# Performance work log

Measured on AMD Instinct MI355X. Metric: run time of the kernel, lower is better.

The kernel has to match this reference:

```python
import jax, jax.numpy as jnp
import numpy as np

D = 512   # d_model
K = 24    # decode steps
B = 8192  # batch


def setup_inputs() -> dict:
    key = jax.random.key(0)
    ks = jax.random.split(key, 10)
    s = 1.0 / np.sqrt(D)
    return {
        "initial": jax.random.normal(ks[0], (B, 1, 1), jnp.float32),
        "encoder_hidden": jax.random.normal(ks[1], (B, D), jnp.float32) * 0.1,
        "encoder_cell": jax.random.normal(ks[2], (B, D), jnp.float32) * 0.1,
        # LSTM params: input dim is 1 (feedback of dense1 output); gate order i,f,g,o (Keras)
        "Wx": jax.random.normal(ks[3], (1, 4 * D), jnp.float32) * s,
        "Wu": jax.random.normal(ks[4], (D, 4 * D), jnp.float32) * s,
        "b": jnp.zeros((4 * D,), jnp.float32),
        "w1": jax.random.normal(ks[5], (D, 1), jnp.float32) * s,
        "b1": jnp.zeros((1,), jnp.float32),
        "w2": jax.random.normal(ks[6], (D, 1), jnp.float32) * s,
        "b2": jnp.zeros((1,), jnp.float32),
    }


def reference(initial, encoder_hidden, encoder_cell, Wx, Wu, b, w1, b1, w2, b2):
    """Autoregressive LSTM decode: step 0 consumes `initial`, then feeds dense1
    output back as the next LSTM input; state carries across all K steps."""

    def step(carry, _):
        x, h, c = carry                      # x:[B,1], h,c:[B,D]
        z = x @ Wx + h @ Wu + b              # [B,4D]
        i, f, g, o = jnp.split(z, 4, axis=-1)
        i = jax.nn.sigmoid(i)
        f = jax.nn.sigmoid(f)
        g = jnp.tanh(g)
        o = jax.nn.sigmoid(o)
        c = f * c + i * g
        h = o * jnp.tanh(c)
        y1 = jax.nn.sigmoid(h @ w1 + b1)     # dense1, feedback input
        y2 = jax.nn.elu(h @ w2 + b2)         # dense2
        return (y1, h, c), (y1, y2)

    x0 = initial[:, 0, :]                    # [B,1]
    _, (ys1, ys2) = jax.lax.scan(step, (x0, encoder_hidden, encoder_cell), None, length=K)
    out1 = jnp.transpose(ys1[..., 0], (1, 0))  # [B,K]
    out2 = jnp.transpose(ys2[..., 0], (1, 0))  # [B,K]
    return out1, out2
```

## Files before the change

kernel.cpp:

```cpp
#include <hip/hip_runtime.h>

#define D_ 512
#define ND_ 2048
#define KS_ 24
#define TB_ 32
#define B_ 8192
#define NU_ 33

typedef __attribute__((ext_vector_type(8))) short short8;
typedef __attribute__((ext_vector_type(16))) float f32x16;
typedef unsigned short u16;

#define SWZ(row, kb) (((row) * 1024) + ((kb) ^ (((row) & 15) << 4)))

__device__ __forceinline__ u16 f2bf(float f) {
  union { float f; unsigned int u; } v; v.f = f;
  unsigned int u = v.u;
  return (u16)((u + 0x7FFFu + ((u >> 16) & 1u)) >> 16);
}

__device__ __forceinline__ float sigm(float x) { return 1.0f / (1.0f + __expf(-x)); }
__device__ __forceinline__ float tanh_(float x) {
  float e = __expf(2.0f * x);
  return (e - 1.0f) / (e + 1.0f);
}

__global__ __launch_bounds__(256) void pack_wu_kernel(const float* __restrict__ Wu,
                                                      const float* __restrict__ Wx,
                                                      const float* __restrict__ b,
                                                      u16* __restrict__ pk) {
  int idx = blockIdx.x * 256 + threadIdx.x;
  int lane = idx & 63;
  int unit = idx >> 6;
  if (unit >= 64 * NU_) return;
  int nt = unit / NU_;
  int un = unit - nt * NU_;
  int col = nt * 32 + (lane & 31);
  u16 t[8] = {0, 0, 0, 0, 0, 0, 0, 0};
  if (un < 32) {
    int k0 = un * 16 + (lane >> 5) * 8;
#pragma unroll
    for (int j = 0; j < 8; ++j) t[j] = f2bf(Wu[(size_t)(k0 + j) * ND_ + col]);
  } else if ((lane >> 5) == 0) {
    t[0] = f2bf(Wx[col]);
    t[1] = f2bf(b[col]);
  }
  int4 w;
  w.x = t[0] | (t[1] << 16); w.y = t[2] | (t[3] << 16);
  w.z = t[4] | (t[5] << 16); w.w = t[6] | (t[7] << 16);
  *reinterpret_cast<int4*>(pk + (size_t)unit * 512 + lane * 8) = w;
}

#define LD8(P, u) (*reinterpret_cast<const short8*>((P) + (size_t)(u) * 512))

#define KSTEP_PASS(CREG, COL, W1V, W2V, P0, P1, P2, P3)                        \
  {                                                                            \
    acc0 = (f32x16){}; acc1 = (f32x16){}; acc2 = (f32x16){}; acc3 = (f32x16){};\
    short8 fA0 = LD8(P0, 0), fA1 = LD8(P1, 0), fA2 = LD8(P2, 0), fA3 = LD8(P3, 0);\
    short8 fB0, fB1, fB2, fB3;                                                 \
    _Pragma("unroll 1")                                                        \
    for (int ks = 0; ks < 32; ks += 2) {                                       \
      fB0 = LD8(P0, ks + 1); fB1 = LD8(P1, ks + 1);                            \
      fB2 = LD8(P2, ks + 1); fB3 = LD8(P3, ks + 1);                            \
      short8 a0 = *reinterpret_cast<const short8*>(&hr[SWZ(l31, ks * 32 + abase)]);\
      acc0 = __builtin_amdgcn_mfma_f32_32x32x16_bf16(a0, fA0, acc0, 0, 0, 0);  \
      acc1 = __builtin_amdgcn_mfma_f32_32x32x16_bf16(a0, fA1, acc1, 0, 0, 0);  \
      acc2 = __builtin_amdgcn_mfma_f32_32x32x16_bf16(a0, fA2, acc2, 0, 0, 0);  \
      acc3 = __builtin_amdgcn_mfma_f32_32x32x16_bf16(a0, fA3, acc3, 0, 0, 0);  \
      fA0 = LD8(P0, ks + 2); fA1 = LD8(P1, ks + 2);  \
      fA2 = LD8(P2, ks + 2); fA3 = LD8(P3, ks + 2);                            \
      short8 a1 = *reinterpret_cast<const short8*>(&hr[SWZ(l31, (ks + 1) * 32 + abase)]);\
      acc0 = __builtin_amdgcn_mfma_f32_32x32x16_bf16(a1, fB0, acc0, 0, 0, 0);  \
      acc1 = __builtin_amdgcn_mfma_f32_32x32x16_bf16(a1, fB1, acc1, 0, 0, 0);  \
      acc2 = __builtin_amdgcn_mfma_f32_32x32x16_bf16(a1, fB2, acc2, 0, 0, 0);  \
      acc3 = __builtin_amdgcn_mfma_f32_32x32x16_bf16(a1, fB3, acc3, 0, 0, 0);  \
    }                                                                          \
    {                   \
      short8 ax = {};                                                          \
      if (lhi == 0) {                                                          \
        ax[0] = (short)f2bf(x_lds[l31]);                                       \
        ax[1] = (short)0x3F80;                                                 \
      }                                                                        \
      acc0 = __builtin_amdgcn_mfma_f32_32x32x16_bf16(ax, fA0, acc0, 0, 0, 0);  \
      acc1 = __builtin_amdgcn_mfma_f32_32x32x16_bf16(ax, fA1, acc1, 0, 0, 0);  \
      acc2 = __builtin_amdgcn_mfma_f32_32x32x16_bf16(ax, fA2, acc2, 0, 0, 0);  \
      acc3 = __builtin_amdgcn_mfma_f32_32x32x16_bf16(ax, fA3, acc3, 0, 0, 0);  \
    }                                                                          \
    _Pragma("unroll")                                                          \
    for (int r = 0; r < 16; ++r) {                                             \
      const int row = (r & 3) + 8 * (r >> 2) + 4 * lhi;                        \
      float ig = sigm(acc0[r]);                                                \
      float fg = sigm(acc1[r]);                                                \
      float gg = tanh_(acc2[r]);                                               \
      float og = sigm(acc3[r]);                                                \
      float cn = fg * CREG[r] + ig * gg;                                       \
      CREG[r] = cn;                                                            \
      float hn = og * tanh_(cn);                                               \
      *reinterpret_cast<u16*>(&hw[SWZ(row, (COL) * 2)]) = f2bf(hn);            \
      y1p[r] += hn * (W1V);                                                    \
      y2p[r] += hn * (W2V);                                                    \
    }                                                                          \
  }

__global__ __launch_bounds__(512, 2) void lstm_kernel(
    const float* __restrict__ initial, const float* __restrict__ enc_h,
    const float* __restrict__ enc_c,
    const float* __restrict__ w1, const float* __restrict__ b1,
    const float* __restrict__ w2, const float* __restrict__ b2,
    const u16* __restrict__ wu, float* __restrict__ out) {
  __shared__ __align__(16) unsigned char hbuf[2][TB_ * 1024];
  __shared__ float x_lds[TB_];
  __shared__ float ly1[8][TB_];
  __shared__ float ly2[8][TB_];

  const int tid = threadIdx.x;
  const int wv  = tid >> 6;
  const int wvu = __builtin_amdgcn_readfirstlane(wv);
  const int l   = tid & 63;
  const int l31 = l & 31;
  const int lhi = l >> 5;
  const int b0  = blockIdx.x * TB_;

  {
    int row = tid >> 4;
    int seg = tid & 15;
    const float* src = enc_h + (size_t)(b0 + row) * D_ + seg * 32;
#pragma unroll
    for (int jb = 0; jb < 4; ++jb) {
      u16 t[8];
#pragma unroll
      for (int j = 0; j < 8; ++j) t[j] = f2bf(src[jb * 8 + j]);
      int kb = seg * 64 + jb * 16;
      int4 w;
      w.x = t[0] | (t[1] << 16); w.y = t[2] | (t[3] << 16);
      w.z = t[4] | (t[5] << 16); w.w = t[6] | (t[7] << 16);
      *reinterpret_cast<int4*>(&hbuf[0][SWZ(row, kb)]) = w;
    }
  }
  if (tid < TB_) x_lds[tid] = initial[b0 + tid];

  const int colA = wvu * 32 + l31;
  const int colB = (8 + wvu) * 32 + l31;
  const float w1vA = w1[colA], w1vB = w1[colB];
  const float w2vA = w2[colA], w2vB = w2[colB];
  const float b1v = b1[0], b2v = b2[0];

  float cregA[16], cregB[16];
#pragma unroll
  for (int r = 0; r < 16; ++r) {
    const int row = (r & 3) + 8 * (r >> 2) + 4 * lhi;
    cregA[r] = enc_c[(size_t)(b0 + row) * D_ + colA];
    cregB[r] = enc_c[(size_t)(b0 + row) * D_ + colB];
  }

  const size_t lofs8 = (size_t)l * 8;
  const u16* pA0 = wu + (size_t)(( 0 + wvu) * NU_) * 512 + lofs8;
  const u16* pA1 = wu + (size_t)((16 + wvu) * NU_) * 512 + lofs8;
  const u16* pA2 = wu + (size_t)((32 + wvu) * NU_) * 512 + lofs8;
  const u16* pA3 = wu + (size_t)((48 + wvu) * NU_) * 512 + lofs8;
  const u16* pB0 = wu + (size_t)(( 8 + wvu) * NU_) * 512 + lofs8;
  const u16* pB1 = wu + (size_t)((24 + wvu) * NU_) * 512 + lofs8;
  const u16* pB2 = wu + (size_t)((40 + wvu) * NU_) * 512 + lofs8;
  const u16* pB3 = wu + (size_t)((56 + wvu) * NU_) * 512 + lofs8;
  const int abase = lhi * 16;

  __syncthreads();

  for (int s = 0; s < KS_; ++s) {
    const unsigned char* hr = hbuf[s & 1];
    unsigned char* hw = hbuf[(s & 1) ^ 1];

    float y1p[16], y2p[16];
#pragma unroll
    for (int r = 0; r < 16; ++r) { y1p[r] = 0.f; y2p[r] = 0.f; }

    f32x16 acc0, acc1, acc2, acc3;
    KSTEP_PASS(cregA, colA, w1vA, w2vA, pA0, pA1, pA2, pA3)
    KSTEP_PASS(cregB, colB, w1vB, w2vB, pB0, pB1, pB2, pB3)

#pragma unroll
    for (int m = 1; m < 32; m <<= 1) {
#pragma unroll
      for (int r = 0; r < 16; ++r) {
        y1p[r] += __shfl_xor(y1p[r], m);
        y2p[r] += __shfl_xor(y2p[r], m);
      }
    }
    if (l31 == 0) {
#pragma unroll
      for (int r = 0; r < 16; ++r) {
        const int row = (r & 3) + 8 * (r >> 2) + 4 * lhi;
        ly1[wvu][row] = y1p[r];
        ly2[wvu][row] = y2p[r];
      }
    }
    __syncthreads();

    if (tid < TB_) {
      float s1 = b1v, s2 = b2v;
#pragma unroll
      for (int wq = 0; wq < 8; ++wq) { s1 += ly1[wq][tid]; s2 += ly2[wq][tid]; }
      float y1 = sigm(s1);
      float y2 = (s2 > 0.f) ? s2 : (__expf(s2) - 1.0f);
      out[(size_t)(b0 + tid) * KS_ + s] = y1;
      out[(size_t)B_ * KS_ + (size_t)(b0 + tid) * KS_ + s] = y2;
      x_lds[tid] = y1;
    }
    __syncthreads();
  }
}

extern "C" void kernel_launch(void* const* d_in, const int* in_sizes, int n_in,
                              void* d_out, int out_size, void* d_ws, size_t ws_size,
                              hipStream_t stream) {
  const float* initial = (const float*)d_in[0];
  const float* enc_h   = (const float*)d_in[1];
  const float* enc_c   = (const float*)d_in[2];
  const float* Wx      = (const float*)d_in[3];
  const float* Wu      = (const float*)d_in[4];
  const float* bias    = (const float*)d_in[5];
  const float* w1      = (const float*)d_in[6];
  const float* b1      = (const float*)d_in[7];
  const float* w2      = (const float*)d_in[8];
  const float* b2      = (const float*)d_in[9];
  u16* pk = (u16*)d_ws;

  pack_wu_kernel<<<528, 256, 0, stream>>>(Wu, Wx, bias, pk);
  lstm_kernel<<<256, 512, 0, stream>>>(initial, enc_h, enc_c, w1, b1,
                                       w2, b2, pk, (float*)d_out);
}
```

Before: 683.0 us.

## Deepen weight prefetch to three stages and overlap next-pass loads with gate math

```diff
diff --git a/kernel.cpp b/kernel.cpp
--- a/kernel.cpp
+++ b/kernel.cpp
@@ -52,54 +52,86 @@
 }
 
 #define LD8(P, u) (*reinterpret_cast<const short8*>((P) + (size_t)(u) * 512))
-
-#define KSTEP_PASS(CREG, COL, W1V, W2V, P0, P1, P2, P3)                        \
+#define AH(ks) (*reinterpret_cast<const short8*>(&hr[SWZ(l31, (ks) * 32 + abase)]))
+#define MFMA_(A, B, C) __builtin_amdgcn_mfma_f32_32x32x16_bf16(A, B, C, 0, 0, 0)
+
+#define KPRO(P0, P1, P2, P3)                                                   \
+    fA0 = LD8(P0, 0); fA1 = LD8(P1, 0); fA2 = LD8(P2, 0); fA3 = LD8(P3, 0);    \
+    fB0 = LD8(P0, 1); fB1 = LD8(P1, 1); fB2 = LD8(P2, 1); fB3 = LD8(P3, 1);    \
+    fC0 = LD8(P0, 2); fC1 = LD8(P1, 2); fC2 = LD8(P2, 2); fC3 = LD8(P3, 2);
+
+#define GATE_REDUCE(CREG, COL, W1V, W2V, PIDX)                                 \
+    _Pragma("unroll")                                                          \
+    for (int rb = 0; rb < 16; rb += 4) {                                       \
+      float y1t[4], y2t[4];                                                    \
+      _Pragma("unroll")                                                        \
+      for (int q = 0; q < 4; ++q) {                                            \
+        const int r = rb + q;                                                  \
+        const int row = q + 8 * (rb >> 2) + 4 * lhi;                           \
+        float ig = sigm(acc0[r]);                                              \
+        float fg = sigm(acc1[r]);                                              \
+        float gg = tanh_(acc2[r]);                                             \
+        float og = sigm(acc3[r]);                                              \
+        float cn = fg * CREG[r] + ig * gg;                                     \
+        CREG[r] = cn;                                                          \
+        float hn = og * tanh_(cn);                                             \
+        *reinterpret_cast<u16*>(&hw[SWZ(row, (COL) * 2)]) = f2bf(hn);          \
+        y1t[q] = hn * (W1V);                                                   \
+        y2t[q] = hn * (W2V);                                                   \
+      }                                                                        \
+      _Pragma("unroll")                                                        \
+      for (int m = 1; m < 32; m <<= 1) {                                       \
+        _Pragma("unroll")                                                      \
+        for (int q = 0; q < 4; ++q) {                                          \
+          y1t[q] += __shfl_xor(y1t[q], m);                                     \
+          y2t[q] += __shfl_xor(y2t[q], m);                                     \
+        }                                                                      \
+      }                                                                        \
+      if (l31 == 0) {                                                          \
+        _Pragma("unroll")                                                      \
+        for (int q = 0; q < 4; ++q) {                                          \
+          const int row = q + 8 * (rb >> 2) + 4 * lhi;                         \
+          ly1[PIDX][wvu][row] = y1t[q];                                        \
+          ly2[PIDX][wvu][row] = y2t[q];                                        \
+        }                                                                      \
+      }                                                                        \
+    }
+
+#define KBODY(CREG, COL, W1V, W2V, P0, P1, P2, P3, PIDX, NEXTPRO)              \
   {                                                                            \
     acc0 = (f32x16){}; acc1 = (f32x16){}; acc2 = (f32x16){}; acc3 = (f32x16){};\
-    short8 fA0 = LD8(P0, 0), fA1 = LD8(P1, 0), fA2 = LD8(P2, 0), fA3 = LD8(P3, 0);\
-    short8 fB0, fB1, fB2, fB3;                                                 \
     _Pragma("unroll 1")                                                        \
-    for (int ks = 0; ks < 32; ks += 2) {                                       \
-      fB0 = LD8(P0, ks + 1); fB1 = LD8(P1, ks + 1);                            \
-      fB2 = LD8(P2, ks + 1); fB3 = LD8(P3, ks + 1);                            \
-      short8 a0 = *reinterpret_cast<const short8*>(&hr[SWZ(l31, ks * 32 + abase)]);\
-      acc0 = __builtin_amdgcn_mfma_f32_32x32x16_bf16(a0, fA0, acc0, 0, 0, 0);  \
-      acc1 = __builtin_amdgcn_mfma_f32_32x32x16_bf16(a0, fA1, acc1, 0, 0, 0);  \
-      acc2 = __builtin_amdgcn_mfma_f32_32x32x16_bf16(a0, fA2, acc2, 0, 0, 0);  \
-      acc3 = __builtin_amdgcn_mfma_f32_32x32x16_bf16(a0, fA3, acc3, 0, 0, 0);  \
-      fA0 = LD8(P0, ks + 2); fA1 = LD8(P1, ks + 2);  \
-      fA2 = LD8(P2, ks + 2); fA3 = LD8(P3, ks + 2);                            \
-      short8 a1 = *reinterpret_cast<const short8*>(&hr[SWZ(l31, (ks + 1) * 32 + abase)]);\
-      acc0 = __builtin_amdgcn_mfma_f32_32x32x16_bf16(a1, fB0, acc0, 0, 0, 0);  \
-      acc1 = __builtin_amdgcn_mfma_f32_32x32x16_bf16(a1, fB1, acc1, 0, 0, 0);  \
-      acc2 = __builtin_amdgcn_mfma_f32_32x32x16_bf16(a1, fB2, acc2, 0, 0, 0);  \
-      acc3 = __builtin_amdgcn_mfma_f32_32x32x16_bf16(a1, fB3, acc3, 0, 0, 0);  \
+    for (int ks = 0; ks < 30; ks += 3) {                                       \
+      short8 a0 = AH(ks);                                                      \
+      acc0 = MFMA_(a0, fA0, acc0); acc1 = MFMA_(a0, fA1, acc1);                \
+      acc2 = MFMA_(a0, fA2, acc2); acc3 = MFMA_(a0, fA3, acc3);                \
+      fA0 = LD8(P0, ks + 3); fA1 = LD8(P1, ks + 3);                            \
+      fA2 = LD8(P2, ks + 3); fA3 = LD8(P3, ks + 3);                            \
+      short8 a1 = AH(ks + 1);                                                  \
+      acc0 = MFMA_(a1, fB0, acc0); acc1 = MFMA_(a1, fB1, acc1);                \
+      acc2 = MFMA_(a1, fB2, acc2); acc3 = MFMA_(a1, fB3, acc3);                \
+      fB0 = LD8(P0, ks + 4); fB1 = LD8(P1, ks + 4);                            \
+      fB2 = LD8(P2, ks + 4); fB3 = LD8(P3, ks + 4);                            \
+      short8 a2 = AH(ks + 2);                                                  \
+      acc0 = MFMA_(a2, fC0, acc0); acc1 = MFMA_(a2, fC1, acc1);                \
+      acc2 = MFMA_(a2, fC2, acc2); acc3 = MFMA_(a2, fC3, acc3);                \
+      fC0 = LD8(P0, ks + 5); fC1 = LD8(P1, ks + 5);                            \
+      fC2 = LD8(P2, ks + 5); fC3 = LD8(P3, ks + 5);                            \
     }                                                                          \
-    {                   \
-      short8 ax = {};                                                          \
-      if (lhi == 0) {                                                          \
-        ax[0] = (short)f2bf(x_lds[l31]);                                       \
-        ax[1] = (short)0x3F80;                                                 \
-      }                                                                        \
-      acc0 = __builtin_amdgcn_mfma_f32_32x32x16_bf16(ax, fA0, acc0, 0, 0, 0);  \
-      acc1 = __builtin_amdgcn_mfma_f32_32x32x16_bf16(ax, fA1, acc1, 0, 0, 0);  \
-      acc2 = __builtin_amdgcn_mfma_f32_32x32x16_bf16(ax, fA2, acc2, 0, 0, 0);  \
-      acc3 = __builtin_amdgcn_mfma_f32_32x32x16_bf16(ax, fA3, acc3, 0, 0, 0);  \
+    {                                                                          \
+      short8 a0 = AH(30);                                                      \
+      acc0 = MFMA_(a0, fA0, acc0); acc1 = MFMA_(a0, fA1, acc1);                \
+      acc2 = MFMA_(a0, fA2, acc2); acc3 = MFMA_(a0, fA3, acc3);                \
+      short8 a1 = AH(31);                                                      \
+      acc0 = MFMA_(a1, fB0, acc0); acc1 = MFMA_(a1, fB1, acc1);                \
+      acc2 = MFMA_(a1, fB2, acc2); acc3 = MFMA_(a1, fB3, acc3);                \
+      short8 ax = {};                     \
+      if (lhi == 0) { ax[0] = (short)f2bf(x_lds[l31]); ax[1] = (short)0x3F80; }\
+      acc0 = MFMA_(ax, fC0, acc0); acc1 = MFMA_(ax, fC1, acc1);                \
+      acc2 = MFMA_(ax, fC2, acc2); acc3 = MFMA_(ax, fC3, acc3);                \
     }                                                                          \
-    _Pragma("unroll")                                                          \
-    for (int r = 0; r < 16; ++r) {                                             \
-      const int row = (r & 3) + 8 * (r >> 2) + 4 * lhi;                        \
-      float ig = sigm(acc0[r]);                                                \
-      float fg = sigm(acc1[r]);                                                \
-      float gg = tanh_(acc2[r]);                                               \
-      float og = sigm(acc3[r]);                                                \
-      float cn = fg * CREG[r] + ig * gg;                                       \
-      CREG[r] = cn;                                                            \
-      float hn = og * tanh_(cn);                                               \
-      *reinterpret_cast<u16*>(&hw[SWZ(row, (COL) * 2)]) = f2bf(hn);            \
-      y1p[r] += hn * (W1V);                                                    \
-      y2p[r] += hn * (W2V);                                                    \
-    }                                                                          \
+    NEXTPRO                                                                    \
+    GATE_REDUCE(CREG, COL, W1V, W2V, PIDX)                                     \
   }
 
 __global__ __launch_bounds__(512, 2) void lstm_kernel(
@@ -110,8 +142,8 @@
     const u16* __restrict__ wu, float* __restrict__ out) {
   __shared__ __align__(16) unsigned char hbuf[2][TB_ * 1024];
   __shared__ float x_lds[TB_];
-  __shared__ float ly1[8][TB_];
-  __shared__ float ly2[8][TB_];
+  __shared__ float ly1[2][8][TB_];
+  __shared__ float ly2[2][8][TB_];
 
   const int tid = threadIdx.x;
   const int wv  = tid >> 6;
@@ -170,36 +202,23 @@
     const unsigned char* hr = hbuf[s & 1];
     unsigned char* hw = hbuf[(s & 1) ^ 1];
 
-    float y1p[16], y2p[16];
-#pragma unroll
-    for (int r = 0; r < 16; ++r) { y1p[r] = 0.f; y2p[r] = 0.f; }
-
+    short8 fA0, fA1, fA2, fA3, fB0, fB1, fB2, fB3, fC0, fC1, fC2, fC3;
     f32x16 acc0, acc1, acc2, acc3;
-    KSTEP_PASS(cregA, colA, w1vA, w2vA, pA0, pA1, pA2, pA3)
-    KSTEP_PASS(cregB, colB, w1vB, w2vB, pB0, pB1, pB2, pB3)
-
-#pragma unroll
-    for (int m = 1; m < 32; m <<= 1) {
-#pragma unroll
-      for (int r = 0; r < 16; ++r) {
-        y1p[r] += __shfl_xor(y1p[r], m);
-        y2p[r] += __shfl_xor(y2p[r], m);
-      }
-    }
-    if (l31 == 0) {
-#pragma unroll
-      for (int r = 0; r < 16; ++r) {
-        const int row = (r & 3) + 8 * (r >> 2) + 4 * lhi;
-        ly1[wvu][row] = y1p[r];
-        ly2[wvu][row] = y2p[r];
-      }
-    }
+
+    KPRO(pA0, pA1, pA2, pA3)
+    KBODY(cregA, colA, w1vA, w2vA, pA0, pA1, pA2, pA3, 0,
+          KPRO(pB0, pB1, pB2, pB3))
+    KBODY(cregB, colB, w1vB, w2vB, pB0, pB1, pB2, pB3, 1, )
+
     __syncthreads();
 
     if (tid < TB_) {
       float s1 = b1v, s2 = b2v;
 #pragma unroll
-      for (int wq = 0; wq < 8; ++wq) { s1 += ly1[wq][tid]; s2 += ly2[wq][tid]; }
+      for (int wq = 0; wq < 8; ++wq) {
+        s1 += ly1[0][wq][tid] + ly1[1][wq][tid];
+        s2 += ly2[0][wq][tid] + ly2[1][wq][tid];
+      }
       float y1 = sigm(s1);
       float y2 = (s2 > 0.f) ? s2 : (__expf(s2) - 1.0f);
       out[(size_t)(b0 + tid) * KS_ + s] = y1;
```

New measurement: 924.1 us. 35.3% more time.

## Quantize LSTM recurrent matmul to int8 MFMA with per-column scales

Applied to the files above, without the earlier changes.

```diff
diff --git a/kernel.cpp b/kernel.cpp
--- a/kernel.cpp
+++ b/kernel.cpp
@@ -5,19 +5,12 @@
 #define KS_ 24
 #define TB_ 32
 #define B_ 8192
-#define NU_ 33
-
-typedef __attribute__((ext_vector_type(8))) short short8;
-typedef __attribute__((ext_vector_type(16))) float f32x16;
-typedef unsigned short u16;
-
-#define SWZ(row, kb) (((row) * 1024) + ((kb) ^ (((row) & 15) << 4)))
-
-__device__ __forceinline__ u16 f2bf(float f) {
-  union { float f; unsigned int u; } v; v.f = f;
-  unsigned int u = v.u;
-  return (u16)((u + 0x7FFFu + ((u >> 16) & 1u)) >> 16);
-}
+#define NUI_ 16
+
+typedef __attribute__((ext_vector_type(4))) int i32x4;
+typedef __attribute__((ext_vector_type(16))) int i32x16;
+
+#define SWZ8(row, kb) (((row) * 512) + ((kb) ^ (((row) & 15) << 4)))
 
 __device__ __forceinline__ float sigm(float x) { return 1.0f / (1.0f + __expf(-x)); }
 __device__ __forceinline__ float tanh_(float x) {
@@ -25,93 +18,116 @@
   return (e - 1.0f) / (e + 1.0f);
 }
 
-__global__ __launch_bounds__(256) void pack_wu_kernel(const float* __restrict__ Wu,
-                                                      const float* __restrict__ Wx,
-                                                      const float* __restrict__ b,
-                                                      u16* __restrict__ pk) {
+__global__ __launch_bounds__(256) void colscale_kernel(const float* __restrict__ Wu,
+                                                       float* __restrict__ sw) {
+  int n = blockIdx.x * 256 + threadIdx.x;
+  float m = 0.f;
+  for (int k = 0; k < D_; ++k) m = fmaxf(m, fabsf(Wu[(size_t)k * ND_ + n]));
+  sw[n] = fmaxf(m, 1e-12f) * (1.0f / 127.0f);
+}
+
+__global__ __launch_bounds__(256) void pack_i8_kernel(const float* __restrict__ Wu,
+                                                      const float* __restrict__ sw,
+                                                      signed char* __restrict__ pk) {
   int idx = blockIdx.x * 256 + threadIdx.x;
   int lane = idx & 63;
   int unit = idx >> 6;
-  if (unit >= 64 * NU_) return;
-  int nt = unit / NU_;
-  int un = unit - nt * NU_;
-  int col = nt * 32 + (lane & 31);
-  u16 t[8] = {0, 0, 0, 0, 0, 0, 0, 0};
-  if (un < 32) {
-    int k0 = un * 16 + (lane >> 5) * 8;
-#pragma unroll
-    for (int j = 0; j < 8; ++j) t[j] = f2bf(Wu[(size_t)(k0 + j) * ND_ + col]);
-  } else if ((lane >> 5) == 0) {
-    t[0] = f2bf(Wx[col]);
-    t[1] = f2bf(b[col]);
-  }
-  int4 w;
-  w.x = t[0] | (t[1] << 16); w.y = t[2] | (t[3] << 16);
-  w.z = t[4] | (t[5] << 16); w.w = t[6] | (t[7] << 16);
-  *reinterpret_cast<int4*>(pk + (size_t)unit * 512 + lane * 8) = w;
-}
-
-#define LD8(P, u) (*reinterpret_cast<const short8*>((P) + (size_t)(u) * 512))
-
-#define KSTEP_PASS(CREG, COL, W1V, W2V, P0, P1, P2, P3)                        \
+  int nt = unit >> 4, ku = unit & 15;
+  int n  = nt * 32 + (lane & 31);
+  int k0 = ku * 32 + (lane >> 5) * 16;
+  float inv = 1.0f / sw[n];
+  unsigned w[4] = {0, 0, 0, 0};
+#pragma unroll
+  for (int e = 0; e < 16; ++e) {
+    float v = rintf(Wu[(size_t)(k0 + e) * ND_ + n] * inv);
+    v = fminf(fmaxf(v, -127.f), 127.f);
+    int qi = (int)v;
+    w[e >> 2] |= (unsigned)(qi & 255) << ((e & 3) * 8);
+  }
+  i32x4 q = {(int)w[0], (int)w[1], (int)w[2], (int)w[3]};
+  *reinterpret_cast<i32x4*>(pk + (size_t)unit * 1024 + lane * 16) = q;
+}
+
+#define LDU(S, u) (*reinterpret_cast<const i32x4*>((S) + (size_t)(u) * 1024 + lofs16))
+#define AH8(ku_) (*reinterpret_cast<const i8x4c*>(&hr[SWZ8(l31, (ku_) * 32 + abase)]))
+#define MFMAI(A, B, C) __builtin_amdgcn_mfma_i32_32x32x32_i8(A, B, C, 0, 0, 0)
+typedef const i32x4 i8x4c;
+
+#define KSTEP_I8(S0, S1, S2, S3)                                               \
   {                                                                            \
-    acc0 = (f32x16){}; acc1 = (f32x16){}; acc2 = (f32x16){}; acc3 = (f32x16){};\
-    short8 fA0 = LD8(P0, 0), fA1 = LD8(P1, 0), fA2 = LD8(P2, 0), fA3 = LD8(P3, 0);\
-    short8 fB0, fB1, fB2, fB3;                                                 \
+    acc0 = (i32x16){}; acc1 = (i32x16){}; acc2 = (i32x16){}; acc3 = (i32x16){};\
+    i32x4 fA0 = LDU(S0, 0), fA1 = LDU(S1, 0), fA2 = LDU(S2, 0), fA3 = LDU(S3, 0);\
+    i32x4 fB0, fB1, fB2, fB3;                                                  \
     _Pragma("unroll 1")                                                        \
-    for (int ks = 0; ks < 32; ks += 2) {                                       \
-      fB0 = LD8(P0, ks + 1); fB1 = LD8(P1, ks + 1);                            \
-      fB2 = LD8(P2, ks + 1); fB3 = LD8(P3, ks + 1);                            \
-      short8 a0 = *reinterpret_cast<const short8*>(&hr[SWZ(l31, ks * 32 + abase)]);\
-      acc0 = __builtin_amdgcn_mfma_f32_32x32x16_bf16(a0, fA0, acc0, 0, 0, 0);  \
-      acc1 = __builtin_amdgcn_mfma_f32_32x32x16_bf16(a0, fA1, acc1, 0, 0, 0);  \
-      acc2 = __builtin_amdgcn_mfma_f32_32x32x16_bf16(a0, fA2, acc2, 0, 0, 0);  \
-      acc3 = __builtin_amdgcn_mfma_f32_32x32x16_bf16(a0, fA3, acc3, 0, 0, 0);  \
-      fA0 = LD8(P0, ks + 2); fA1 = LD8(P1, ks + 2);  \
-      fA2 = LD8(P2, ks + 2); fA3 = LD8(P3, ks + 2);                            \
-      short8 a1 = *reinterpret_cast<const short8*>(&hr[SWZ(l31, (ks + 1) * 32 + abase)]);\
-      acc0 = __builtin_amdgcn_mfma_f32_32x32x16_bf16(a1, fB0, acc0, 0, 0, 0);  \
-      acc1 = __builtin_amdgcn_mfma_f32_32x32x16_bf16(a1, fB1, acc1, 0, 0, 0);  \
-      acc2 = __builtin_amdgcn_mfma_f32_32x32x16_bf16(a1, fB2, acc2, 0, 0, 0);  \
-      acc3 = __builtin_amdgcn_mfma_f32_32x32x16_bf16(a1, fB3, acc3, 0, 0, 0);  \
+    for (int ku = 0; ku < 14; ku += 2) {                                       \
+      fB0 = LDU(S0, ku + 1); fB1 = LDU(S1, ku + 1);                            \
+      fB2 = LDU(S2, ku + 1); fB3 = LDU(S3, ku + 1);                            \
+      i32x4 a0 = AH8(ku);                                                      \
+      acc0 = MFMAI(a0, fA0, acc0); acc1 = MFMAI(a0, fA1, acc1);                \
+      acc2 = MFMAI(a0, fA2, acc2); acc3 = MFMAI(a0, fA3, acc3);                \
+      fA0 = LDU(S0, ku + 2); fA1 = LDU(S1, ku + 2);                            \
+      fA2 = LDU(S2, ku + 2); fA3 = LDU(S3, ku + 2);                            \
+      i32x4 a1 = AH8(ku + 1);                                                  \
+      acc0 = MFMAI(a1, fB0, acc0); acc1 = MFMAI(a1, fB1, acc1);                \
+      acc2 = MFMAI(a1, fB2, acc2); acc3 = MFMAI(a1, fB3, acc3);                \
     }                                                                          \
-    {                   \
-      short8 ax = {};                                                          \
-      if (lhi == 0) {                                                          \
-        ax[0] = (short)f2bf(x_lds[l31]);                                       \
-        ax[1] = (short)0x3F80;                                                 \
-      }                                                                        \
-      acc0 = __builtin_amdgcn_mfma_f32_32x32x16_bf16(ax, fA0, acc0, 0, 0, 0);  \
-      acc1 = __builtin_amdgcn_mfma_f32_32x32x16_bf16(ax, fA1, acc1, 0, 0, 0);  \
-      acc2 = __builtin_amdgcn_mfma_f32_32x32x16_bf16(ax, fA2, acc2, 0, 0, 0);  \
-      acc3 = __builtin_amdgcn_mfma_f32_32x32x16_bf16(ax, fA3, acc3, 0, 0, 0);  \
+    {                                                                          \
+      fB0 = LDU(S0, 15); fB1 = LDU(S1, 15);                                    \
+      fB2 = LDU(S2, 15); fB3 = LDU(S3, 15);                                    \
+      i32x4 a0 = AH8(14);                                                      \
+      acc0 = MFMAI(a0, fA0, acc0); acc1 = MFMAI(a0, fA1, acc1);                \
+      acc2 = MFMAI(a0, fA2, acc2); acc3 = MFMAI(a0, fA3, acc3);                \
+      i32x4 a1 = AH8(15);                                                      \
+      acc0 = MFMAI(a1, fB0, acc0); acc1 = MFMAI(a1, fB1, acc1);                \
+      acc2 = MFMAI(a1, fB2, acc2); acc3 = MFMAI(a1, fB3, acc3);                \
     }                                                                          \
+  }
+
+#define GATEPH(CREG, COL, W1V, W2V)                                            \
+  {                                                                            \
+    const float swi = sw_l[COL],        swf = sw_l[512 + COL];                 \
+    const float swg = sw_l[1024 + COL], swo = sw_l[1536 + COL];                \
+    const float wxi = wx_l[COL],        wxf = wx_l[512 + COL];                 \
+    const float wxg = wx_l[1024 + COL], wxo = wx_l[1536 + COL];                \
+    const float bbi = bb_l[COL],        bbf = bb_l[512 + COL];                 \
+    const float bbg = bb_l[1024 + COL], bbo = bb_l[1536 + COL];                \
     _Pragma("unroll")                                                          \
     for (int r = 0; r < 16; ++r) {                                             \
       const int row = (r & 3) + 8 * (r >> 2) + 4 * lhi;                        \
-      float ig = sigm(acc0[r]);                                                \
-      float fg = sigm(acc1[r]);                                                \
-      float gg = tanh_(acc2[r]);                                               \
-      float og = sigm(acc3[r]);                                                \
+      const float xv = x_lds[row];                                             \
+      float zi = swi * (float)acc0[r] + xv * wxi + bbi;                        \
+      float zf = swf * (float)acc1[r] + xv * wxf + bbf;                        \
+      float zg = swg * (float)acc2[r] + xv * wxg + bbg;                        \
+      float zo = swo * (float)acc3[r] + xv * wxo + bbo;                        \
+      float ig = sigm(zi);                                                     \
+      float fg = sigm(zf);                                                     \
+      float gg = tanh_(zg);                                                    \
+      float og = sigm(zo);                                                     \
       float cn = fg * CREG[r] + ig * gg;                                       \
       CREG[r] = cn;                                                            \
       float hn = og * tanh_(cn);                                               \
-      *reinterpret_cast<u16*>(&hw[SWZ(row, (COL) * 2)]) = f2bf(hn);            \
+      hw[SWZ8(row, COL)] = (signed char)__float2int_rn(hn * 127.0f);           \
       y1p[r] += hn * (W1V);                                                    \
       y2p[r] += hn * (W2V);                                                    \
     }                                                                          \
   }
 
-__global__ __launch_bounds__(512, 2) void lstm_kernel(
+__global__ __launch_bounds__(512) void lstm_kernel(
     const float* __restrict__ initial, const float* __restrict__ enc_h,
-    const float* __restrict__ enc_c,
+    const float* __restrict__ enc_c, const float* __restrict__ Wx,
+    const float* __restrict__ bias,
     const float* __restrict__ w1, const float* __restrict__ b1,
     const float* __restrict__ w2, const float* __restrict__ b2,
-    const u16* __restrict__ wu, float* __restrict__ out) {
-  __shared__ __align__(16) unsigned char hbuf[2][TB_ * 1024];
+    const signed char* __restrict__ pk, const float* __restrict__ swg_,
+    float* __restrict__ out) {
+  __shared__ __align__(16) signed char hbuf[2][TB_ * 512];
+  __shared__ float sw_l[ND_];
+  __shared__ float wx_l[ND_];
+  __shared__ float bb_l[ND_];
   __shared__ float x_lds[TB_];
   __shared__ float ly1[8][TB_];
   __shared__ float ly2[8][TB_];
+  __shared__ float ystg[2][TB_][KS_];
 
   const int tid = threadIdx.x;
   const int wv  = tid >> 6;
@@ -121,26 +137,37 @@
   const int lhi = l >> 5;
   const int b0  = blockIdx.x * TB_;
 
+#pragma unroll
+  for (int j = 0; j < 4; ++j) {
+    int n = tid + 512 * j;
+    sw_l[n] = swg_[n] * (1.0f / 127.0f);
+    wx_l[n] = Wx[n];
+    bb_l[n] = bias[n];
+  }
+
   {
     int row = tid >> 4;
     int seg = tid & 15;
     const float* src = enc_h + (size_t)(b0 + row) * D_ + seg * 32;
-#pragma unroll
-    for (int jb = 0; jb < 4; ++jb) {
-      u16 t[8];
-#pragma unroll
-      for (int j = 0; j < 8; ++j) t[j] = f2bf(src[jb * 8 + j]);
-      int kb = seg * 64 + jb * 16;
-      int4 w;
-      w.x = t[0] | (t[1] << 16); w.y = t[2] | (t[3] << 16);
-      w.z = t[4] | (t[5] << 16); w.w = t[6] | (t[7] << 16);
-      *reinterpret_cast<int4*>(&hbuf[0][SWZ(row, kb)]) = w;
+    const int m = (row & 15) << 4;
+#pragma unroll
+    for (int half = 0; half < 2; ++half) {
+      unsigned w[4] = {0, 0, 0, 0};
+#pragma unroll
+      for (int i = 0; i < 16; ++i) {
+        float v = rintf(src[half * 16 + i] * 127.0f);
+        v = fminf(fmaxf(v, -127.f), 127.f);
+        w[i >> 2] |= (unsigned)((int)v & 255) << ((i & 3) * 8);
+      }
+      i32x4 q = {(int)w[0], (int)w[1], (int)w[2], (int)w[3]};
+      int addr = row * 512 + ((seg * 32 + half * 16) ^ m);
+      *reinterpret_cast<i32x4*>(&hbuf[0][addr]) = q;
     }
   }
   if (tid < TB_) x_lds[tid] = initial[b0 + tid];
 
   const int colA = wvu * 32 + l31;
-  const int colB = (8 + wvu) * 32 + l31;
+  const int colB = 256 + colA;
   const float w1vA = w1[colA], w1vB = w1[colB];
   const float w2vA = w2[colA], w2vB = w2[colB];
   const float b1v = b1[0], b2v = b2[0];
@@ -153,30 +180,32 @@
     cregB[r] = enc_c[(size_t)(b0 + row) * D_ + colB];
   }
 
-  const size_t lofs8 = (size_t)l * 8;
-  const u16* pA0 = wu + (size_t)(( 0 + wvu) * NU_) * 512 + lofs8;
-  const u16* pA1 = wu + (size_t)((16 + wvu) * NU_) * 512 + lofs8;
-  const u16* pA2 = wu + (size_t)((32 + wvu) * NU_) * 512 + lofs8;
-  const u16* pA3 = wu + (size_t)((48 + wvu) * NU_) * 512 + lofs8;
-  const u16* pB0 = wu + (size_t)(( 8 + wvu) * NU_) * 512 + lofs8;
-  const u16* pB1 = wu + (size_t)((24 + wvu) * NU_) * 512 + lofs8;
-  const u16* pB2 = wu + (size_t)((40 + wvu) * NU_) * 512 + lofs8;
-  const u16* pB3 = wu + (size_t)((56 + wvu) * NU_) * 512 + lofs8;
+  const signed char* sA0 = pk + (size_t)(( 0 + wvu) * NUI_) * 1024;
+  const signed char* sA1 = pk + (size_t)((16 + wvu) * NUI_) * 1024;
+  const signed char* sA2 = pk + (size_t)((32 + wvu) * NUI_) * 1024;
+  const signed char* sA3 = pk + (size_t)((48 + wvu) * NUI_) * 1024;
+  const signed char* sB0 = pk + (size_t)(( 8 + wvu) * NUI_) * 1024;
+  const signed char* sB1 = pk + (size_t)((24 + wvu) * NUI_) * 1024;
+  const signed char* sB2 = pk + (size_t)((40 + wvu) * NUI_) * 1024;
+  const signed char* sB3 = pk + (size_t)((56 + wvu) * NUI_) * 1024;
+  const size_t lofs16 = (size_t)l * 16;
   const int abase = lhi * 16;
 
   __syncthreads();
 
   for (int s = 0; s < KS_; ++s) {
-    const unsigned char* hr = hbuf[s & 1];
-    unsigned char* hw = hbuf[(s & 1) ^ 1];
+    const signed char* hr = hbuf[s & 1];
+    signed char* hw = hbuf[(s & 1) ^ 1];
 
     float y1p[16], y2p[16];
 #pragma unroll
     for (int r = 0; r < 16; ++r) { y1p[r] = 0.f; y2p[r] = 0.f; }
 
-    f32x16 acc0, acc1, acc2, acc3;
-    KSTEP_PASS(cregA, colA, w1vA, w2vA, pA0, pA1, pA2, pA3)
-    KSTEP_PASS(cregB, colB, w1vB, w2vB, pB0, pB1, pB2, pB3)
+    i32x16 acc0, acc1, acc2, acc3;
+    KSTEP_I8(sA0, sA1, sA2, sA3)
+    GATEPH(cregA, colA, w1vA, w2vA)
+    KSTEP_I8(sB0, sB1, sB2, sB3)
+    GATEPH(cregB, colB, w1vB, w2vB)
 
 #pragma unroll
     for (int m = 1; m < 32; m <<= 1) {
@@ -202,11 +231,19 @@
       for (int wq = 0; wq < 8; ++wq) { s1 += ly1[wq][tid]; s2 += ly2[wq][tid]; }
       float y1 = sigm(s1);
       float y2 = (s2 > 0.f) ? s2 : (__expf(s2) - 1.0f);
-      out[(size_t)(b0 + tid) * KS_ + s] = y1;
-      out[(size_t)B_ * KS_ + (size_t)(b0 + tid) * KS_ + s] = y2;
+      ystg[0][tid][s] = y1;
+      ystg[1][tid][s] = y2;
       x_lds[tid] = y1;
     }
     __syncthreads();
+  }
+
+  for (int i = tid; i < 2 * TB_ * KS_; i += 512) {
+    int which = i / (TB_ * KS_);
+    int rem = i - which * (TB_ * KS_);
+    int row = rem / KS_;
+    int k = rem - row * KS_;
+    out[(size_t)which * B_ * KS_ + (size_t)(b0 + row) * KS_ + k] = ystg[which][row][k];
   }
 }
 
@@ -223,9 +260,11 @@
   const float* b1      = (const float*)d_in[7];
   const float* w2      = (const float*)d_in[8];
   const float* b2      = (const float*)d_in[9];
-  u16* pk = (u16*)d_ws;
-
-  pack_wu_kernel<<<528, 256, 0, stream>>>(Wu, Wx, bias, pk);
-  lstm_kernel<<<256, 512, 0, stream>>>(initial, enc_h, enc_c, w1, b1,
-                                       w2, b2, pk, (float*)d_out);
-}
+  signed char* pk = (signed char*)d_ws;
+  float* sw = (float*)((char*)d_ws + (1 << 20));
+
+  colscale_kernel<<<8, 256, 0, stream>>>(Wu, sw);
+  pack_i8_kernel<<<256, 256, 0, stream>>>(Wu, sw, pk);
+  lstm_kernel<<<256, 512, 0, stream>>>(initial, enc_h, enc_c, Wx, bias,
+                                       w1, b1, w2, b2, pk, sw, (float*)d_out);
+}
```

Result: slower. 809.7 us (+18.5%).
